# Kernel tuning notes

Measured on AMD Instinct MI355X. Metric: run time of the kernel, lower is better.

The kernel has to match this reference:

```python
import jax, jax.numpy as jnp
import numpy as np
from jax import lax

LIN_DIMS = [(3200, 2048), (2048, 1024), (1024, 512), (512, 256), (256, 128),
            (128, 64), (64, 32), (32, 16), (16, 8), (8, 4), (4, 2), (2, 1)]
BN_EPS = 1e-5


def _conv(x, w, b):
    y = lax.conv_general_dilated(x, w, window_strides=(3, 3),
                                 padding=((1, 1), (1, 1)),
                                 dimension_numbers=('NCHW', 'OIHW', 'NCHW'))
    return y + b.reshape(1, -1, 1, 1)


def _bn(x, g, b):
    # training-mode BatchNorm2d: biased batch statistics over (N, H, W)
    m = jnp.mean(x, axis=(0, 2, 3), keepdims=True)
    v = jnp.var(x, axis=(0, 2, 3), keepdims=True)
    return (x - m) * lax.rsqrt(v + BN_EPS) * g.reshape(1, -1, 1, 1) + b.reshape(1, -1, 1, 1)


def setup_inputs() -> dict:
    key = jax.random.key(0)
    ks = iter(jax.random.split(key, 64))
    d = {}
    d['x'] = jax.random.normal(next(ks), (64, 512, 40, 40), jnp.float32)
    d['conv1_w'] = jax.random.normal(next(ks), (256, 512, 3, 3), jnp.float32) / np.sqrt(512 * 9)
    d['conv1_b'] = jnp.zeros((256,), jnp.float32)
    d['bn1_g'] = jnp.ones((256,), jnp.float32)
    d['bn1_b'] = jnp.zeros((256,), jnp.float32)
    d['conv2_w'] = jax.random.normal(next(ks), (128, 256, 3, 3), jnp.float32) / np.sqrt(256 * 9)
    d['conv2_b'] = jnp.zeros((128,), jnp.float32)
    d['bn2_g'] = jnp.ones((128,), jnp.float32)
    d['bn2_b'] = jnp.zeros((128,), jnp.float32)
    for i, (fin, fout) in enumerate(LIN_DIMS):
        d[f'w{i+3}'] = jax.random.normal(next(ks), (fout, fin), jnp.float32) / np.sqrt(fin)
        d[f'b{i+3}'] = jax.random.normal(next(ks), (fout,), jnp.float32) * 0.01
    return d


def reference(x, conv1_w, conv1_b, bn1_g, bn1_b, conv2_w, conv2_b, bn2_g, bn2_b,
              w3, b3, w4, b4, w5, b5, w6, b6, w7, b7, w8, b8, w9, b9,
              w10, b10, w11, b11, w12, b12, w13, b13, w14, b14):
    h = _bn(_conv(x, conv1_w, conv1_b), bn1_g, bn1_b)          # [B,256,14,14]
    h = _bn(_conv(h, conv2_w, conv2_b), bn2_g, bn2_b)          # [B,128,5,5]
    h = h.reshape(h.shape[0], 3200)
    for w, b in [(w3, b3), (w4, b4), (w5, b5), (w6, b6), (w7, b7), (w8, b8),
                 (w9, b9), (w10, b10), (w11, b11), (w12, b12), (w13, b13), (w14, b14)]:
        h = h @ w.T + b
    return jax.nn.sigmoid(h)                                   # [B,1]
```

## Files before the change

### kernel.cpp

```cpp
#include <hip/hip_runtime.h>
#include <cstdint>
#include <cstddef>

typedef short bf16x8 __attribute__((ext_vector_type(8)));
typedef float f32x4 __attribute__((ext_vector_type(4)));

__device__ __forceinline__ unsigned short f2bf(float f) {
  union { float f; unsigned u; } v; v.f = f;
  unsigned r = v.u + 0x7fffu + ((v.u >> 16) & 1u);
  return (unsigned short)(r >> 16);
}

#define GLOAD_LDS16(gp, lp)                                            \
  __builtin_amdgcn_global_load_lds(                                    \
      (const __attribute__((address_space(1))) void*)(const void*)(gp),\
      (__attribute__((address_space(3))) void*)(void*)(lp), 16, 0, 0)

__global__ __launch_bounds__(256) void cast2(const float* __restrict__ w1,
                                             const float* __restrict__ w2,
                                             unsigned short* __restrict__ W1b,
                                             unsigned short* __restrict__ W2b) {
  int i = blockIdx.x * 256 + threadIdx.x;
  const float* src; unsigned short* dst; int j;
  if (i < 294912) { src = w1; dst = W1b; j = i; }
  else if (i < 368640) { src = w2; dst = W2b; j = i - 294912; }
  else return;
  float4 v = ((const float4*)src)[j];
  ushort4 o;
  o.x = f2bf(v.x); o.y = f2bf(v.y); o.z = f2bf(v.z); o.w = f2bf(v.w);
  ((ushort4*)dst)[j] = o;
}

__global__ __launch_bounds__(256) void im2col1(const float* __restrict__ x,
                                               unsigned short* __restrict__ A1) {
  __shared__ float buf[64 * 126];
  int t = threadIdx.x;
  int cc = blockIdx.x, oh = blockIdx.y, n = blockIdx.z;
  int ci0 = cc * 64;
  int ih0 = oh * 3 - 1;
  for (int rowid = t; rowid < 192; rowid += 256) {
    int c = rowid / 3, r = rowid - c * 3;
    buf[c * 126 + r * 42 + 0] = 0.f;
    buf[c * 126 + r * 42 + 41] = 0.f;
  }
  for (int idx = t; idx < 1920; idx += 256) {
    int row = idx / 10, ch = idx - row * 10;
    int c = row / 3, r = row - c * 3;
    int ih = ih0 + r;
    float4 v = make_float4(0.f, 0.f, 0.f, 0.f);
    if ((unsigned)ih < 40u)
      v = *(const float4*)(x + (((size_t)n * 512 + ci0 + c) * 40 + ih) * 40 + ch * 4);
    float* dst = buf + c * 126 + r * 42 + 1 + ch * 4;
    dst[0] = v.x; dst[1] = v.y; dst[2] = v.z; dst[3] = v.w;
  }
  __syncthreads();
  for (int idx = t; idx < 2016; idx += 256) {
    int ow = idx / 144, q4 = idx - ow * 144;
    int kk = q4 * 4;
    unsigned short vv[4];
#pragma unroll
    for (int j = 0; j < 4; ++j) {
      int k = kk + j;
      int c = k / 9, rr = k - c * 9;
      int kh = rr / 3, kw = rr - kh * 3;
      vv[j] = f2bf(buf[c * 126 + kh * 42 + 3 * ow + kw]);
    }
    ushort4 o; o.x = vv[0]; o.y = vv[1]; o.z = vv[2]; o.w = vv[3];
    *(ushort4*)(A1 + ((size_t)(n * 196 + oh * 14 + ow)) * 4608 + cc * 576 + kk) = o;
  }
}

__global__ __launch_bounds__(256) void im2col2(const float* __restrict__ C1,
                                               const float* __restrict__ SUM1,
                                               const float* __restrict__ SQ1,
                                               const float* __restrict__ g,
                                               const float* __restrict__ b,
                                               unsigned short* __restrict__ A2) {
  unsigned idx = blockIdx.x * 256u + threadIdx.x;
  unsigned m = idx / 2304u;
  unsigned k = idx - m * 2304u;
  unsigned n = m / 25u, sp = m - n * 25u;
  unsigned oh = sp / 5u, ow = sp - oh * 5u;
  int ci = (int)(k / 9u); int r = (int)k - ci * 9;
  int kh = r / 3, kw = r - kh * 3;
  int ih = (int)oh * 3 - 1 + kh, iw = (int)ow * 3 - 1 + kw;
  float v = 0.f;
  if ((unsigned)ih < 14u && (unsigned)iw < 14u) {
    float mean = SUM1[ci] * (1.f / 12544.f);
    float var = SQ1[ci] * (1.f / 12544.f) - mean * mean;
    float sc = g[ci] / sqrtf(var + 1e-5f);
    float sh = b[ci] - mean * sc;
    v = C1[((size_t)n * 196 + ih * 14 + iw) * 256 + ci] * sc + sh;
  }
  A2[idx] = f2bf(v);
}

template <int BN>
__global__ __launch_bounds__(256) void gemm_bf16(const unsigned short* __restrict__ A,
                                                 const unsigned short* __restrict__ B,
                                                 float* __restrict__ Cp,
                                                 int M, int N, int K, int k_chunk) {
  __shared__ __align__(16) unsigned short As[64 * 32];
  __shared__ __align__(16) unsigned short Bs[BN * 32];
  constexpr int WN = BN / 2;
  constexpr int NT = WN / 16;
  int m0 = blockIdx.x * 64;
  int n0 = blockIdx.y * BN;
  int kb = blockIdx.z;
  Cp += (size_t)kb * M * N;
  int k_begin = kb * k_chunk;
  int t = threadIdx.x;
  int q = (t & 63) >> 4, mr = t & 15;
  int wm = ((t >> 6) & 1) * 32;
  int wn = (t >> 7) * WN;
  f32x4 acc[2][NT] = {};

  for (int k0 = k_begin; k0 < k_begin + k_chunk; k0 += 32) {
    __syncthreads();
    GLOAD_LDS16(A + (size_t)(m0 + (t >> 2)) * K + k0 + (t & 3) * 8, As + t * 8);
#pragma unroll
    for (int i = 0; i < BN / 64; ++i) {
      int c = t + i * 256;
      GLOAD_LDS16(B + (size_t)(n0 + (c >> 2)) * K + k0 + (c & 3) * 8, Bs + c * 8);
    }
    __syncthreads();
    bf16x8 af[2];
#pragma unroll
    for (int s = 0; s < 2; ++s)
      af[s] = *((const bf16x8*)(As + (wm + s * 16 + mr) * 32 + q * 8));
#pragma unroll
    for (int nt = 0; nt < NT; ++nt) {
      bf16x8 bfr = *((const bf16x8*)(Bs + (wn + nt * 16 + mr) * 32 + q * 8));
#pragma unroll
      for (int s = 0; s < 2; ++s)
        acc[s][nt] = __builtin_amdgcn_mfma_f32_16x16x32_bf16(af[s], bfr, acc[s][nt], 0, 0, 0);
    }
  }
#pragma unroll
  for (int s = 0; s < 2; ++s)
#pragma unroll
    for (int nt = 0; nt < NT; ++nt)
#pragma unroll
      for (int r = 0; r < 4; ++r)
        Cp[(size_t)(m0 + wm + s * 16 + q * 4 + r) * N + n0 + wn + nt * 16 + mr] = acc[s][nt][r];
}

template <int KS>
__global__ void reduce_stats(const float* __restrict__ Cp, float* __restrict__ C,
                             float* __restrict__ sum, float* __restrict__ sumsq,
                             int rowsPerBlock, int ncols, int MN) {
  int c = threadIdx.x;
  int r0 = blockIdx.x * rowsPerBlock;
  float s = 0.f, s2 = 0.f;
  for (int r = 0; r < rowsPerBlock; ++r) {
    size_t off = (size_t)(r0 + r) * ncols + c;
    float v = 0.f;
#pragma unroll
    for (int k = 0; k < KS; ++k) v += Cp[(size_t)k * MN + off];
    C[off] = v;
    s += v; s2 += v * v;
  }
  atomicAdd(&sum[c], s);
  atomicAdd(&sumsq[c], s2);
}

__global__ void mlp_head(const float* w14, const float* b14,
                         const float* w13, const float* b13,
                         const float* w12, const float* b12,
                         const float* w11, const float* b11,
                         const float* w10, const float* b10,
                         const float* w9,  const float* b9,
                         const float* w8,  const float* b8,
                         const float* w7,  const float* b7,
                         float* __restrict__ r_out, float* __restrict__ c_out) {
  __shared__ float ra[256], rb[256];
  int t = threadIdx.x;
  float cs = 0.f;
  if (t < 2) ra[t] = w14[t];
  if (t == 0) cs = b14[0];
  __syncthreads();
  const float* Ws[7] = {w13, w12, w11, w10, w9, w8, w7};
  const float* Bs[7] = {b13, b12, b11, b10, b9, b8, b7};
  const int fouts[7] = {2, 4, 8, 16, 32, 64, 128};
  float* cur = ra; float* nxt = rb;
  for (int s = 0; s < 7; ++s) {
    int fo = fouts[s], fi = fo * 2;
    if (t == 0) {
      float d = 0.f;
      for (int i = 0; i < fo; ++i) d += cur[i] * Bs[s][i];
      cs += d;
    }
    if (t < fi) {
      float a = 0.f;
      const float* W = Ws[s];
      for (int i = 0; i < fo; ++i) a += cur[i] * W[i * fi + t];
      nxt[t] = a;
    }
    __syncthreads();
    float* tmp = cur; cur = nxt; nxt = tmp;
  }
  r_out[t] = cur[t];
  if (t == 0) c_out[0] = cs;
}

__global__ void mlp_stage(const float* __restrict__ W, const float* __restrict__ bt,
                          const float* __restrict__ r_in, const float* __restrict__ c_in,
                          float* __restrict__ r_out, float* __restrict__ c_out,
                          int fin, int fout) {
  __shared__ float red[256];
  int t = threadIdx.x;
  int jl = t & 31, ig = t >> 5;
  int j = blockIdx.x * 32 + jl;
  int chunk = fout >> 3;
  int i0 = ig * chunk;
  float acc = 0.f;
  for (int i = i0; i < i0 + chunk; ++i)
    acc += r_in[i] * W[(size_t)i * fin + j];
  red[t] = acc;
  __syncthreads();
  if (ig == 0) {
    float s = 0.f;
#pragma unroll
    for (int u = 0; u < 8; ++u) s += red[u * 32 + jl];
    r_out[j] = s;
  }
  if (blockIdx.x == 0) {
    __syncthreads();
    float p = 0.f;
    for (int i = t; i < fout; i += 256) p += r_in[i] * bt[i];
    red[t] = p;
    __syncthreads();
    for (int s = 128; s > 0; s >>= 1) {
      if (t < s) red[t] += red[t + s];
      __syncthreads();
    }
    if (t == 0) c_out[0] = red[0] + c_in[0];
  }
}

__global__ void final_k(const float* __restrict__ C2, const float* __restrict__ SUM2,
                        const float* __restrict__ SQ2, const float* __restrict__ g2,
                        const float* __restrict__ b2, const float* __restrict__ r,
                        const float* __restrict__ c_in, float* __restrict__ out) {
  int n = blockIdx.x;
  int t = threadIdx.x;
  float acc = 0.f;
  for (int j = t; j < 3200; j += 256) {
    int c = j / 25, sp = j - c * 25;
    float mean = SUM2[c] * (1.f / 1600.f);
    float var = SQ2[c] * (1.f / 1600.f) - mean * mean;
    float sc = g2[c] / sqrtf(var + 1e-5f);
    float sh = b2[c] - mean * sc;
    float v = C2[((size_t)n * 25 + sp) * 128 + c] * sc + sh;
    acc += v * r[j];
  }
  __shared__ float red[256];
  red[t] = acc;
  __syncthreads();
  for (int s = 128; s > 0; s >>= 1) {
    if (t < s) red[t] += red[t + s];
    __syncthreads();
  }
  if (t == 0) {
    float z = red[0] + c_in[0];
    out[n] = 1.f / (1.f + expf(-z));
  }
}

static constexpr size_t OFF_A1   = 0;
static constexpr size_t OFF_C1   = 0;
static constexpr size_t OFF_A2   = 16777216;
static constexpr size_t OFF_C2P  = 33554432;
static constexpr size_t OFF_C2   = 41943040;
static constexpr size_t OFF_W1B  = 115605504;
static constexpr size_t OFF_W2B  = 117964800;
static constexpr size_t OFF_STATS= 118554624;
static constexpr size_t OFF_RA   = 118558720;
static constexpr size_t OFF_RB   = 118571776;
static constexpr size_t OFF_CA   = 118584832;
static constexpr size_t OFF_CB   = 118584960;
static constexpr size_t OFF_C1P  = 118585344;

extern "C" void kernel_launch(void* const* d_in, const int* in_sizes, int n_in,
                              void* d_out, int out_size, void* d_ws, size_t ws_size,
                              hipStream_t stream) {
  const float* x   = (const float*)d_in[0];
  const float* w1  = (const float*)d_in[1];
  const float* g1  = (const float*)d_in[3];
  const float* bb1 = (const float*)d_in[4];
  const float* w2  = (const float*)d_in[5];
  const float* g2  = (const float*)d_in[7];
  const float* bb2 = (const float*)d_in[8];

  char* ws = (char*)d_ws;
  unsigned short* A1  = (unsigned short*)(ws + OFF_A1);
  float*          C1  = (float*)(ws + OFF_C1);
  unsigned short* A2  = (unsigned short*)(ws + OFF_A2);
  float*          C2P = (float*)(ws + OFF_C2P);
  float*          C2  = (float*)(ws + OFF_C2);
  unsigned short* W1b = (unsigned short*)(ws + OFF_W1B);
  unsigned short* W2b = (unsigned short*)(ws + OFF_W2B);
  float* SUM1 = (float*)(ws + OFF_STATS);
  float* SQ1  = (float*)(ws + OFF_STATS + 1024);
  float* SUM2 = (float*)(ws + OFF_STATS + 2048);
  float* SQ2  = (float*)(ws + OFF_STATS + 3072);
  float* RA   = (float*)(ws + OFF_RA);
  float* RB   = (float*)(ws + OFF_RB);
  float* CA   = (float*)(ws + OFF_CA);
  float* CB   = (float*)(ws + OFF_CB);
  float* C1P  = (float*)(ws + OFF_C1P);

  const size_t cpart = 12845056;
  int ks1 = (ws_size >= OFF_C1P + 4 * cpart) ? 4
          : (ws_size >= OFF_C1P + 2 * cpart) ? 2 : 1;

  hipMemsetAsync(ws + OFF_STATS, 0, 4096, stream);

  cast2<<<1440, 256, 0, stream>>>(w1, w2, W1b, W2b);

  im2col1<<<dim3(8, 14, 64), 256, 0, stream>>>(x, A1);
  gemm_bf16<128><<<dim3(196, 2, ks1), 256, 0, stream>>>(A1, W1b, C1P, 12544, 256, 4608,
                                                        4608 / ks1);
  if (ks1 == 4)
    reduce_stats<4><<<392, 256, 0, stream>>>(C1P, C1, SUM1, SQ1, 32, 256, 3211264);
  else if (ks1 == 2)
    reduce_stats<2><<<392, 256, 0, stream>>>(C1P, C1, SUM1, SQ1, 32, 256, 3211264);
  else
    reduce_stats<1><<<392, 256, 0, stream>>>(C1P, C1, SUM1, SQ1, 32, 256, 3211264);

  im2col2<<<14400, 256, 0, stream>>>(C1, SUM1, SQ1, g1, bb1, A2);
  gemm_bf16<64><<<dim3(25, 2, 8), 256, 0, stream>>>(A2, W2b, C2P, 1600, 128, 2304, 288);
  reduce_stats<8><<<100, 128, 0, stream>>>(C2P, C2, SUM2, SQ2, 16, 128, 204800);

  mlp_head<<<1, 256, 0, stream>>>(
      (const float*)d_in[31], (const float*)d_in[32],
      (const float*)d_in[29], (const float*)d_in[30],
      (const float*)d_in[27], (const float*)d_in[28],
      (const float*)d_in[25], (const float*)d_in[26],
      (const float*)d_in[23], (const float*)d_in[24],
      (const float*)d_in[21], (const float*)d_in[22],
      (const float*)d_in[19], (const float*)d_in[20],
      (const float*)d_in[17], (const float*)d_in[18],
      RA, CA);
  mlp_stage<<<16, 256, 0, stream>>>((const float*)d_in[15], (const float*)d_in[16],
                                    RA, CA, RB, CB, 512, 256);
  mlp_stage<<<32, 256, 0, stream>>>((const float*)d_in[13], (const float*)d_in[14],
                                    RB, CB, RA, CA, 1024, 512);
  mlp_stage<<<64, 256, 0, stream>>>((const float*)d_in[11], (const float*)d_in[12],
                                    RA, CA, RB, CB, 2048, 1024);
  mlp_stage<<<100, 256, 0, stream>>>((const float*)d_in[9], (const float*)d_in[10],
                                     RB, CB, RA, CA, 3200, 2048);

  final_k<<<64, 256, 0, stream>>>(C2, SUM2, SQ2, g2, bb2, RA, CA, (float*)d_out);
}
```

Before: 849.1 us.

## Fuse conv1 split-K reduction with im2col2 and fold BN1 into conv2 weights

Conv1's split-K partial sums are now reduced directly inside a new kernel that also accumulates BN1 statistics and writes the bf16 im2col rows for conv2. This drops the separate materialised C1 tensor and the standalone im2col2 pass. BN1's per-channel scale is folded into conv2's bf16 weights, and its shift becomes a per-position bias term that respects padding and is added during the conv2 reduction. The conv1 GEMM moves to a 128x64 tile with a fixed split-K of 2, which raises per-block reuse. In exchange it adds a prep kernel, fixes a larger workspace layout, and rounds the scaled weights to bf16.

```diff
diff --git a/kernel.cpp b/kernel.cpp
--- a/kernel.cpp
+++ b/kernel.cpp
@@ -16,19 +16,13 @@
       (const __attribute__((address_space(1))) void*)(const void*)(gp),\
       (__attribute__((address_space(3))) void*)(void*)(lp), 16, 0, 0)
 
-__global__ __launch_bounds__(256) void cast2(const float* __restrict__ w1,
-                                             const float* __restrict__ w2,
-                                             unsigned short* __restrict__ W1b,
-                                             unsigned short* __restrict__ W2b) {
+__global__ __launch_bounds__(256) void cast1(const float* __restrict__ w1,
+                                             unsigned short* __restrict__ W1b) {
   int i = blockIdx.x * 256 + threadIdx.x;
-  const float* src; unsigned short* dst; int j;
-  if (i < 294912) { src = w1; dst = W1b; j = i; }
-  else if (i < 368640) { src = w2; dst = W2b; j = i - 294912; }
-  else return;
-  float4 v = ((const float4*)src)[j];
+  float4 v = ((const float4*)w1)[i];
   ushort4 o;
   o.x = f2bf(v.x); o.y = f2bf(v.y); o.z = f2bf(v.z); o.w = f2bf(v.w);
-  ((ushort4*)dst)[j] = o;
+  ((ushort4*)W1b)[i] = o;
 }
 
 __global__ __launch_bounds__(256) void im2col1(const float* __restrict__ x,
@@ -70,74 +64,53 @@
   }
 }
 
-__global__ __launch_bounds__(256) void im2col2(const float* __restrict__ C1,
-                                               const float* __restrict__ SUM1,
-                                               const float* __restrict__ SQ1,
-                                               const float* __restrict__ g,
-                                               const float* __restrict__ b,
-                                               unsigned short* __restrict__ A2) {
-  unsigned idx = blockIdx.x * 256u + threadIdx.x;
-  unsigned m = idx / 2304u;
-  unsigned k = idx - m * 2304u;
-  unsigned n = m / 25u, sp = m - n * 25u;
-  unsigned oh = sp / 5u, ow = sp - oh * 5u;
-  int ci = (int)(k / 9u); int r = (int)k - ci * 9;
-  int kh = r / 3, kw = r - kh * 3;
-  int ih = (int)oh * 3 - 1 + kh, iw = (int)ow * 3 - 1 + kw;
-  float v = 0.f;
-  if ((unsigned)ih < 14u && (unsigned)iw < 14u) {
-    float mean = SUM1[ci] * (1.f / 12544.f);
-    float var = SQ1[ci] * (1.f / 12544.f) - mean * mean;
-    float sc = g[ci] / sqrtf(var + 1e-5f);
-    float sh = b[ci] - mean * sc;
-    v = C1[((size_t)n * 196 + ih * 14 + iw) * 256 + ci] * sc + sh;
-  }
-  A2[idx] = f2bf(v);
-}
-
-template <int BN>
+template <int BM, int BN>
 __global__ __launch_bounds__(256) void gemm_bf16(const unsigned short* __restrict__ A,
                                                  const unsigned short* __restrict__ B,
                                                  float* __restrict__ Cp,
                                                  int M, int N, int K, int k_chunk) {
-  __shared__ __align__(16) unsigned short As[64 * 32];
+  __shared__ __align__(16) unsigned short As[BM * 32];
   __shared__ __align__(16) unsigned short Bs[BN * 32];
-  constexpr int WN = BN / 2;
-  constexpr int NT = WN / 16;
-  int m0 = blockIdx.x * 64;
+  constexpr int MT = BM / 32;
+  constexpr int NT = BN / 32;
+  int m0 = blockIdx.x * BM;
   int n0 = blockIdx.y * BN;
-  int kb = blockIdx.z;
-  Cp += (size_t)kb * M * N;
-  int k_begin = kb * k_chunk;
+  Cp += (size_t)blockIdx.z * M * N;
+  int k_begin = blockIdx.z * k_chunk;
   int t = threadIdx.x;
   int q = (t & 63) >> 4, mr = t & 15;
-  int wm = ((t >> 6) & 1) * 32;
-  int wn = (t >> 7) * WN;
-  f32x4 acc[2][NT] = {};
+  int wm = ((t >> 6) & 1) * (BM / 2);
+  int wn = (t >> 7) * (BN / 2);
+  f32x4 acc[MT][NT] = {};
 
   for (int k0 = k_begin; k0 < k_begin + k_chunk; k0 += 32) {
     __syncthreads();
-    GLOAD_LDS16(A + (size_t)(m0 + (t >> 2)) * K + k0 + (t & 3) * 8, As + t * 8);
+#pragma unroll
+    for (int i = 0; i < BM / 64; ++i) {
+      int c = t + i * 256;
+      GLOAD_LDS16(A + (size_t)(m0 + (c >> 2)) * K + k0 + (c & 3) * 8, As + c * 8);
+    }
 #pragma unroll
     for (int i = 0; i < BN / 64; ++i) {
       int c = t + i * 256;
       GLOAD_LDS16(B + (size_t)(n0 + (c >> 2)) * K + k0 + (c & 3) * 8, Bs + c * 8);
     }
     __syncthreads();
-    bf16x8 af[2];
-#pragma unroll
-    for (int s = 0; s < 2; ++s)
+    bf16x8 af[MT], bfr[NT];
+#pragma unroll
+    for (int s = 0; s < MT; ++s)
       af[s] = *((const bf16x8*)(As + (wm + s * 16 + mr) * 32 + q * 8));
 #pragma unroll
-    for (int nt = 0; nt < NT; ++nt) {
-      bf16x8 bfr = *((const bf16x8*)(Bs + (wn + nt * 16 + mr) * 32 + q * 8));
-#pragma unroll
-      for (int s = 0; s < 2; ++s)
-        acc[s][nt] = __builtin_amdgcn_mfma_f32_16x16x32_bf16(af[s], bfr, acc[s][nt], 0, 0, 0);
-    }
-  }
-#pragma unroll
-  for (int s = 0; s < 2; ++s)
+    for (int nt = 0; nt < NT; ++nt)
+      bfr[nt] = *((const bf16x8*)(Bs + (wn + nt * 16 + mr) * 32 + q * 8));
+#pragma unroll
+    for (int nt = 0; nt < NT; ++nt)
+#pragma unroll
+      for (int s = 0; s < MT; ++s)
+        acc[s][nt] = __builtin_amdgcn_mfma_f32_16x16x32_bf16(af[s], bfr[nt], acc[s][nt], 0, 0, 0);
+  }
+#pragma unroll
+  for (int s = 0; s < MT; ++s)
 #pragma unroll
     for (int nt = 0; nt < NT; ++nt)
 #pragma unroll
@@ -145,23 +118,93 @@
         Cp[(size_t)(m0 + wm + s * 16 + q * 4 + r) * N + n0 + wn + nt * 16 + mr] = acc[s][nt][r];
 }
 
-template <int KS>
-__global__ void reduce_stats(const float* __restrict__ Cp, float* __restrict__ C,
-                             float* __restrict__ sum, float* __restrict__ sumsq,
-                             int rowsPerBlock, int ncols, int MN) {
+__global__ __launch_bounds__(256) void reduce1_scatter(const float* __restrict__ C1P,
+                                                       unsigned short* __restrict__ A2,
+                                                       float* __restrict__ SUM1,
+                                                       float* __restrict__ SQ1) {
+  __shared__ __align__(16) unsigned short row[2304];
+  int m2 = blockIdx.x, t = threadIdx.x;
+  int n = m2 / 25, sp = m2 - n * 25;
+  int oh = sp / 5, ow = sp - oh * 5;
+  float s = 0.f, s2 = 0.f;
+#pragma unroll
+  for (int r = 0; r < 9; ++r) {
+    int kh = r / 3, kw = r - kh * 3;
+    int ih = 3 * oh - 1 + kh, iw = 3 * ow - 1 + kw;
+    float v = 0.f;
+    if (ih >= 0 && iw >= 0) {
+      size_t off = (size_t)(n * 196 + ih * 14 + iw) * 256 + t;
+      v = C1P[off] + C1P[3211264 + off];
+      s += v; s2 += v * v;
+    }
+    row[t * 9 + r] = f2bf(v);
+  }
+  atomicAdd(&SUM1[t], s);
+  atomicAdd(&SQ1[t], s2);
+  __syncthreads();
+  uint4* dst = (uint4*)(A2 + (size_t)m2 * 2304);
+  const uint4* src = (const uint4*)row;
+  for (int i = t; i < 288; i += 256) dst[i] = src[i];
+}
+
+__global__ __launch_bounds__(256) void prep2(const float* __restrict__ w2,
+                                             const float* __restrict__ g1,
+                                             const float* __restrict__ b1,
+                                             const float* __restrict__ SUM1,
+                                             const float* __restrict__ SQ1,
+                                             unsigned short* __restrict__ W2s,
+                                             float* __restrict__ T) {
+  int bid = blockIdx.x, t = threadIdx.x;
+  if (bid < 1152) {
+    int idx = bid * 256 + t;
+    int k2 = idx % 2304; int ci = k2 / 9;
+    float mean = SUM1[ci] * (1.f / 12544.f);
+    float var = SQ1[ci] * (1.f / 12544.f) - mean * mean;
+    float sc = g1[ci] * rsqrtf(var + 1e-5f);
+    W2s[idx] = f2bf(w2[idx] * sc);
+  } else {
+    int b2 = bid - 1152;
+    int sp = b2 >> 7, n = b2 & 127;
+    int oh = sp / 5, ow = sp - oh * 5;
+    float p = 0.f;
+    for (int k2 = t; k2 < 2304; k2 += 256) {
+      int ci = k2 / 9, r = k2 - ci * 9;
+      int ih = 3 * oh - 1 + r / 3, iw = 3 * ow - 1 + r % 3;
+      if (ih >= 0 && iw >= 0) {
+        float mean = SUM1[ci] * (1.f / 12544.f);
+        float var = SQ1[ci] * (1.f / 12544.f) - mean * mean;
+        float sc = g1[ci] * rsqrtf(var + 1e-5f);
+        float sh = b1[ci] - mean * sc;
+        p += w2[n * 2304 + k2] * sh;
+      }
+    }
+    __shared__ float red[256];
+    red[t] = p; __syncthreads();
+    for (int s = 128; s > 0; s >>= 1) {
+      if (t < s) red[t] += red[t + s];
+      __syncthreads();
+    }
+    if (t == 0) T[sp * 128 + n] = red[0];
+  }
+}
+
+__global__ void reduce2_k(const float* __restrict__ C2P, const float* __restrict__ T,
+                          float* __restrict__ C2, float* __restrict__ SUM2,
+                          float* __restrict__ SQ2) {
   int c = threadIdx.x;
-  int r0 = blockIdx.x * rowsPerBlock;
+  int r0 = blockIdx.x * 16;
   float s = 0.f, s2 = 0.f;
-  for (int r = 0; r < rowsPerBlock; ++r) {
-    size_t off = (size_t)(r0 + r) * ncols + c;
-    float v = 0.f;
-#pragma unroll
-    for (int k = 0; k < KS; ++k) v += Cp[(size_t)k * MN + off];
-    C[off] = v;
+  for (int r = 0; r < 16; ++r) {
+    int m = r0 + r, sp = m % 25;
+    size_t off = (size_t)m * 128 + c;
+    float v = T[sp * 128 + c];
+#pragma unroll
+    for (int k = 0; k < 8; ++k) v += C2P[(size_t)k * 204800 + off];
+    C2[off] = v;
     s += v; s2 += v * v;
   }
-  atomicAdd(&sum[c], s);
-  atomicAdd(&sumsq[c], s2);
+  atomicAdd(&SUM2[c], s);
+  atomicAdd(&SQ2[c], s2);
 }
 
 __global__ void mlp_head(const float* w14, const float* b14,
@@ -268,18 +311,18 @@
 }
 
 static constexpr size_t OFF_A1   = 0;
-static constexpr size_t OFF_C1   = 0;
-static constexpr size_t OFF_A2   = 16777216;
-static constexpr size_t OFF_C2P  = 33554432;
-static constexpr size_t OFF_C2   = 41943040;
-static constexpr size_t OFF_W1B  = 115605504;
-static constexpr size_t OFF_W2B  = 117964800;
-static constexpr size_t OFF_STATS= 118554624;
-static constexpr size_t OFF_RA   = 118558720;
-static constexpr size_t OFF_RB   = 118571776;
-static constexpr size_t OFF_CA   = 118584832;
-static constexpr size_t OFF_CB   = 118584960;
-static constexpr size_t OFF_C1P  = 118585344;
+static constexpr size_t OFF_C1P  = 115605504;
+static constexpr size_t OFF_A2   = 141295616;
+static constexpr size_t OFF_C2P  = 148668416;
+static constexpr size_t OFF_C2   = 155222016;
+static constexpr size_t OFF_W1B  = 156041216;
+static constexpr size_t OFF_W2S  = 158400512;
+static constexpr size_t OFF_T    = 158990336;
+static constexpr size_t OFF_STATS= 159003136;
+static constexpr size_t OFF_RA   = 159007232;
+static constexpr size_t OFF_RB   = 159020288;
+static constexpr size_t OFF_CA   = 159033344;
+static constexpr size_t OFF_CB   = 159033472;
 
 extern "C" void kernel_launch(void* const* d_in, const int* in_sizes, int n_in,
                               void* d_out, int out_size, void* d_ws, size_t ws_size,
@@ -294,12 +337,13 @@
 
   char* ws = (char*)d_ws;
   unsigned short* A1  = (unsigned short*)(ws + OFF_A1);
-  float*          C1  = (float*)(ws + OFF_C1);
+  float*          C1P = (float*)(ws + OFF_C1P);
   unsigned short* A2  = (unsigned short*)(ws + OFF_A2);
   float*          C2P = (float*)(ws + OFF_C2P);
   float*          C2  = (float*)(ws + OFF_C2);
   unsigned short* W1b = (unsigned short*)(ws + OFF_W1B);
-  unsigned short* W2b = (unsigned short*)(ws + OFF_W2B);
+  unsigned short* W2s = (unsigned short*)(ws + OFF_W2S);
+  float*          T   = (float*)(ws + OFF_T);
   float* SUM1 = (float*)(ws + OFF_STATS);
   float* SQ1  = (float*)(ws + OFF_STATS + 1024);
   float* SUM2 = (float*)(ws + OFF_STATS + 2048);
@@ -308,29 +352,20 @@
   float* RB   = (float*)(ws + OFF_RB);
   float* CA   = (float*)(ws + OFF_CA);
   float* CB   = (float*)(ws + OFF_CB);
-  float* C1P  = (float*)(ws + OFF_C1P);
-
-  const size_t cpart = 12845056;
-  int ks1 = (ws_size >= OFF_C1P + 4 * cpart) ? 4
-          : (ws_size >= OFF_C1P + 2 * cpart) ? 2 : 1;
 
   hipMemsetAsync(ws + OFF_STATS, 0, 4096, stream);
 
-  cast2<<<1440, 256, 0, stream>>>(w1, w2, W1b, W2b);
+  cast1<<<1152, 256, 0, stream>>>(w1, W1b);
 
   im2col1<<<dim3(8, 14, 64), 256, 0, stream>>>(x, A1);
-  gemm_bf16<128><<<dim3(196, 2, ks1), 256, 0, stream>>>(A1, W1b, C1P, 12544, 256, 4608,
-                                                        4608 / ks1);
-  if (ks1 == 4)
-    reduce_stats<4><<<392, 256, 0, stream>>>(C1P, C1, SUM1, SQ1, 32, 256, 3211264);
-  else if (ks1 == 2)
-    reduce_stats<2><<<392, 256, 0, stream>>>(C1P, C1, SUM1, SQ1, 32, 256, 3211264);
-  else
-    reduce_stats<1><<<392, 256, 0, stream>>>(C1P, C1, SUM1, SQ1, 32, 256, 3211264);
-
-  im2col2<<<14400, 256, 0, stream>>>(C1, SUM1, SQ1, g1, bb1, A2);
-  gemm_bf16<64><<<dim3(25, 2, 8), 256, 0, stream>>>(A2, W2b, C2P, 1600, 128, 2304, 288);
-  reduce_stats<8><<<100, 128, 0, stream>>>(C2P, C2, SUM2, SQ2, 16, 128, 204800);
+  gemm_bf16<128, 64><<<dim3(98, 4, 2), 256, 0, stream>>>(A1, W1b, C1P, 12544, 256, 4608, 2304);
+
+  reduce1_scatter<<<1600, 256, 0, stream>>>(C1P, A2, SUM1, SQ1);
+
+  prep2<<<4352, 256, 0, stream>>>(w2, g1, bb1, SUM1, SQ1, W2s, T);
+
+  gemm_bf16<64, 64><<<dim3(25, 2, 8), 256, 0, stream>>>(A2, W2s, C2P, 1600, 128, 2304, 288);
+  reduce2_k<<<100, 128, 0, stream>>>(C2P, T, C2, SUM2, SQ2);
 
   mlp_head<<<1, 256, 0, stream>>>(
       (const float*)d_in[31], (const float*)d_in[32],
```

New measurement: 867.0 us. 1.02x slower.
